# Optimization experiments

Hardware: AMD Instinct MI355X
Metric: run time of the kernel (lower is better)

The kernel has to match this reference:

```python
import jax, jax.numpy as jnp
import numpy as np

NUM_RBF = 16
TOP_K = 30
LOWER = 0.0
UPPER = 20.0
MAX_REL = 32  # PositionalEncodings max_relative_feature


def layer_norm(x, g, b, eps=1e-5):
    m = jnp.mean(x, -1, keepdims=True)
    v = jnp.var(x, -1, keepdims=True)
    return (x - m) / jnp.sqrt(v + eps) * g + b


def rbf(D):
    # exp(-((D - mu)/sigma)^2), mu = linspace(LOWER, UPPER, NUM_RBF)
    mu = jnp.linspace(LOWER, UPPER, NUM_RBF)
    sigma = (UPPER - LOWER) / NUM_RBF
    return jnp.exp(-(((D[..., None] - mu) / sigma) ** 2))


def setup_inputs() -> dict:
    key = jax.random.key(0)
    ks = jax.random.split(key, 6)
    B, L, A = 1, 1536, 14
    x = jax.random.normal(ks[0], (B, L, A, 3), jnp.float32) * 5.0
    S = jax.random.randint(ks[1], (B, L), 0, 21)
    mask = jnp.ones((B, L), jnp.float32)
    atom14_mask = jnp.ones((B, L, A), jnp.float32)
    R_idx = jnp.broadcast_to(jnp.arange(L, dtype=jnp.int32), (B, L))
    chain_labels = jnp.zeros((B, L), jnp.int32)
    protein_mpnn_feat = jax.random.normal(ks[2], (B, L, 128), jnp.float32)
    W_pos = jax.random.normal(ks[3], (2 * MAX_REL + 2, 16), jnp.float32) * 0.12
    b_pos = jnp.zeros((16,), jnp.float32)
    W_edge = jax.random.normal(ks[4], (16 + NUM_RBF * 14 * 14, 128), jnp.float32) * 0.018
    gamma_e = jnp.ones((128,), jnp.float32)
    beta_e = jnp.zeros((128,), jnp.float32)
    W_node = jax.random.normal(ks[5], (21 + 128, 128), jnp.float32) * 0.08
    gamma_n = jnp.ones((128,), jnp.float32)
    beta_n = jnp.zeros((128,), jnp.float32)
    return dict(x=x, mask=mask, atom14_mask=atom14_mask,
                protein_mpnn_feat=protein_mpnn_feat,
                W_pos=W_pos, b_pos=b_pos, W_edge=W_edge, gamma_e=gamma_e,
                beta_e=beta_e, W_node=W_node, gamma_n=gamma_n, beta_n=beta_n,
                S=S, R_idx=R_idx, chain_labels=chain_labels)


def reference(x, mask, atom14_mask, protein_mpnn_feat,
              W_pos, b_pos, W_edge, gamma_e, beta_e,
              W_node, gamma_n, beta_n, S, R_idx, chain_labels):
    B, L, A, _ = x.shape  # A = 14
    X_m = atom14_mask * mask[:, :, None]          # [B,L,14]
    Ca = x[:, :, 1]                                # CA_idx = 1

    # ---- _dist: masked pairwise CA distances + kNN topk (smallest) ----
    m2 = mask[:, None, :] * mask[:, :, None]       # [B,L,L]
    dX = Ca[:, None, :, :] - Ca[:, :, None, :]
    D = m2 * jnp.sqrt(jnp.sum(dX ** 2, -1) + 1e-6)
    D_max = jnp.max(D, -1, keepdims=True)
    D_adjust = D + (1.0 - m2) * D_max
    _, E_idx = jax.lax.top_k(-D_adjust, TOP_K)     # [B,L,K] smallest distances

    bidx = jnp.arange(B)[:, None, None]
    # gather neighbor atom coords / masks (all_coords_list == x in atom14 order)
    Xg = x[bidx, E_idx]                            # [B,L,K,14,3]
    Xm_g = X_m[bidx, E_idx]                        # [B,L,K,14]

    # ---- 14x14 pairwise atom RBFs to neighbors, fused/vectorized ----
    # Dp[b,l,k,i,j] = ||x[b,l,i] - x[b,E_idx[b,l,k],j]||
    Dp = jnp.sqrt(jnp.sum((x[:, :, None, :, None, :] - Xg[:, :, :, None, :, :]) ** 2, -1) + 1e-6)
    R = rbf(Dp)                                    # [B,L,K,14,14,16]
    R = R * X_m[:, :, None, :, None, None] * Xm_g[:, :, :, None, :, None]
    # torch loop cats atom_1-major, atom_2, then rbf bins -> same as reshape
    RBF_all = R.reshape(B, L, TOP_K, A * A * NUM_RBF)  # [B,L,K,3136]

    # ---- positional encodings ----
    offset = R_idx[:, :, None] - R_idx[:, None, :]           # [B,L,L]
    offset_g = jnp.take_along_axis(offset, E_idx, axis=2)    # [B,L,K]
    d_chains = (chain_labels[:, :, None] == chain_labels[:, None, :]).astype(jnp.int32)
    E_chains = jnp.take_along_axis(d_chains, E_idx, axis=2)  # [B,L,K]
    d = jnp.clip(offset_g + MAX_REL, 0, 2 * MAX_REL) * E_chains \
        + (1 - E_chains) * (2 * MAX_REL + 1)
    E_pos = jax.nn.one_hot(d, 2 * MAX_REL + 2, dtype=x.dtype) @ W_pos + b_pos

    # ---- edge embedding ----
    E = jnp.concatenate([E_pos, RBF_all], -1) @ W_edge       # [B,L,K,128]
    E = layer_norm(E, gamma_e, beta_e)

    # ---- node embedding ----
    V = jnp.concatenate([jax.nn.one_hot(S, 21, dtype=x.dtype), protein_mpnn_feat], -1) @ W_node
    V = layer_norm(V, gamma_n, beta_n)

    return (V, E, E_idx, x)
```

## Files before the change

### kernel.cpp

```cpp
#include <hip/hip_runtime.h>
#include <hip/hip_bf16.h>
#include <hip/hip_fp16.h>
#include <math.h>

#define LL 1536
#define NA 14
#define TOPK 30
#define KDIM 3152
#define KPAD 3200
#define NCHUNK 50

#define TOPK_BLKS 384
#define CONV_BLKS 100
#define NODE_BLKS 384
#define PREP_BLKS (TOPK_BLKS + CONV_BLKS + NODE_BLKS)

#define EDGE_BLKS 768

typedef __attribute__((ext_vector_type(8))) short bf16x8;
typedef __attribute__((ext_vector_type(4))) float f32x4;

static __device__ __forceinline__ float fexp2(float f) {
    return __builtin_amdgcn_exp2f(f);
}

static __device__ __forceinline__ unsigned cvt_pk_bf16(float lo, float hi) {
    unsigned r;
    asm("v_cvt_pk_bf16_f32 %0, %1, %2" : "=v"(r) : "v"(lo), "v"(hi));
    return r;
}

static __device__ __forceinline__ unsigned long long u64min(
    unsigned long long a, unsigned long long b) { return a < b ? a : b; }
static __device__ __forceinline__ unsigned long long u64max(
    unsigned long long a, unsigned long long b) { return a < b ? b : a; }

#define ASYNC16(ldsp, gp)                                                     \
    __builtin_amdgcn_global_load_lds(                                         \
        (const __attribute__((address_space(1))) void*)(gp),                  \
        (__attribute__((address_space(3))) void*)(ldsp), 16, 0, 0)

static __device__ __forceinline__ void build_rbf(
    ushort* dst, float4 xi4, float4 xj4,
    const float (&cA)[7], const float (&cB)[7])
{
    float dx = xi4.x - xj4.x, dy = xi4.y - xj4.y, dz = xi4.z - xj4.z;
    float dd = sqrtf(dx * dx + dy * dy + dz * dz + 1e-6f);
    dd = fminf(dd, 27.f);
    float coef = xi4.w * xj4.w;
    float w = fexp2(dd * 2.46219921f);
    float ev[16];
    float s8 = dd - 10.66666667f;
    ev[0] = fexp2(-0.92332483f * dd * dd) * coef;
    ev[8] = fexp2(-0.92332483f * s8 * s8) * coef;
    #pragma unroll
    for (int j = 1; j <= 7; ++j) {
        ev[j]     = ev[j - 1]     * w * cA[j - 1];
        ev[8 + j] = ev[8 + j - 1] * w * cB[j - 1];
    }
    union { unsigned u[8]; uint4 q[2]; } o;
    #pragma unroll
    for (int c = 0; c < 8; ++c) o.u[c] = cvt_pk_bf16(ev[2 * c], ev[2 * c + 1]);
    *(uint4*)&dst[0] = o.q[0];
    *(uint4*)&dst[8] = o.q[1];
}

__global__ __launch_bounds__(256) void prep_kernel(
    const float* __restrict__ x, const float* __restrict__ mask,
    const float* __restrict__ feat,
    const float* __restrict__ W_edge, ushort* __restrict__ Wt,
    const float* __restrict__ W_node, const float* __restrict__ gamma_n,
    const float* __restrict__ beta_n, const int* __restrict__ S,
    float* __restrict__ V, float* __restrict__ out_idx, float* __restrict__ out_x)
{
    __shared__ __align__(16) char sm[24576];
    const int blk = blockIdx.x;
    const int tid = threadIdx.x;

    if (blk < TOPK_BLKS) {
        float* ca  = (float*)sm;
        float* msk = (float*)sm + 4608;
        for (int t = tid; t < LL; t += 256) {
            msk[t] = mask[t];
            ca[t * 3 + 0] = x[t * 42 + 3];
            ca[t * 3 + 1] = x[t * 42 + 4];
            ca[t * 3 + 2] = x[t * 42 + 5];
        }
        __syncthreads();

        const int lane = tid & 63;
        const int i = blk * 4 + (tid >> 6);
        const float cix = ca[i * 3 + 0], ciy = ca[i * 3 + 1], ciz = ca[i * 3 + 2];
        const float mi = msk[i];

        float d[24], m2a[24];
        float lmax = 0.f;
        #pragma unroll
        for (int c = 0; c < 24; ++c) {
            int j = lane + c * 64;
            float dx = ca[j * 3 + 0] - cix;
            float dy = ca[j * 3 + 1] - ciy;
            float dz = ca[j * 3 + 2] - ciz;
            float m2 = mi * msk[j];
            float D = m2 * sqrtf(dx * dx + dy * dy + dz * dz + 1e-6f);
            d[c] = D; m2a[c] = m2;
            lmax = fmaxf(lmax, D);
        }
        #pragma unroll
        for (int m = 1; m < 64; m <<= 1) lmax = fmaxf(lmax, __shfl_xor(lmax, m));

        unsigned long long key[24];
        #pragma unroll
        for (int c = 0; c < 24; ++c) {
            float adj = d[c] + (1.f - m2a[c]) * lmax;
            key[c] = ((unsigned long long)__float_as_uint(adj) << 32)
                   | (unsigned)(lane + c * 64);
        }

        for (int t = 0; t < TOPK; t += 2) {
            unsigned long long p[12], q[12];
            #pragma unroll
            for (int c = 0; c < 12; ++c) {
                unsigned long long a = key[2 * c], b = key[2 * c + 1];
                p[c] = u64min(a, b); q[c] = u64max(a, b);
            }
            #pragma unroll
            for (int c = 0; c < 6; ++c) {
                unsigned long long hp = u64min(p[2 * c], p[2 * c + 1]);
                unsigned long long hq = u64min(u64max(p[2 * c], p[2 * c + 1]),
                                               u64min(q[2 * c], q[2 * c + 1]));
                p[c] = hp; q[c] = hq;
            }
            #pragma unroll
            for (int c = 0; c < 3; ++c) {
                unsigned long long hp = u64min(p[2 * c], p[2 * c + 1]);
                unsigned long long hq = u64min(u64max(p[2 * c], p[2 * c + 1]),
                                               u64min(q[2 * c], q[2 * c + 1]));
                p[c] = hp; q[c] = hq;
            }
            unsigned long long P = u64min(p[0], p[1]);
            unsigned long long Q = u64min(u64max(p[0], p[1]), u64min(q[0], q[1]));
            unsigned long long P2 = u64min(P, p[2]);
            unsigned long long Q2 = u64min(u64max(P, p[2]), u64min(Q, q[2]));
            #pragma unroll
            for (int m = 1; m < 64; m <<= 1) {
                unsigned long long op = __shfl_xor(P2, m);
                unsigned long long oq = __shfl_xor(Q2, m);
                unsigned long long np = u64min(P2, op);
                unsigned long long nq = u64min(u64max(P2, op), u64min(Q2, oq));
                P2 = np; Q2 = nq;
            }
            if (lane == 0) {
                out_idx[i * TOPK + t]     = (float)(unsigned)(P2 & 0xffffffffu);
                out_idx[i * TOPK + t + 1] = (float)(unsigned)(Q2 & 0xffffffffu);
            }
            #pragma unroll
            for (int c = 0; c < 24; ++c)
                if (key[c] == P2 || key[c] == Q2) key[c] = ~0ull;
        }
        for (int t = lane; t < 42; t += 64) out_x[i * 42 + t] = x[i * 42 + t];

    } else if (blk < TOPK_BLKS + CONV_BLKS) {
        int cb = blk - TOPK_BLKS;
        int k0 = (cb % 50) * 64, n0 = (cb / 50) * 64;
        float (*tile)[65] = (float (*)[65])sm;
        #pragma unroll
        for (int r = 0; r < 16; ++r) {
            int idx = r * 256 + tid;
            int kl = idx >> 6, nl = idx & 63;
            int k = k0 + kl;
            tile[nl][kl] = (k < KDIM) ? W_edge[k * 128 + n0 + nl] : 0.f;
        }
        __syncthreads();
        #pragma unroll
        for (int r = 0; r < 8; ++r) {
            int idx = r * 256 + tid;
            int nl = idx >> 5, kp = (idx & 31) * 2;
            unsigned pk = cvt_pk_bf16(tile[nl][kp], tile[nl][kp + 1]);
            *(unsigned*)&Wt[(size_t)(n0 + nl) * KPAD + k0 + kp] = pk;
        }

    } else {
        int nb = blk - TOPK_BLKS - CONV_BLKS;
        float* f = (float*)sm;
        const int w = tid >> 6, lane = tid & 63;
        const int i = nb * 4 + w;
        f[w * 128 + lane] = feat[i * 128 + lane];
        f[w * 128 + 64 + lane] = feat[i * 128 + 64 + lane];
        __syncthreads();
        int s = S[i];
        float a0 = W_node[s * 128 + lane];
        float a1 = W_node[s * 128 + 64 + lane];
        #pragma unroll 8
        for (int c = 0; c < 128; ++c) {
            float fc = f[w * 128 + c];
            a0 = fmaf(fc, W_node[(21 + c) * 128 + lane], a0);
            a1 = fmaf(fc, W_node[(21 + c) * 128 + 64 + lane], a1);
        }
        float ss = a0 + a1, qq = a0 * a0 + a1 * a1;
        #pragma unroll
        for (int m = 1; m < 64; m <<= 1) {
            ss += __shfl_xor(ss, m);
            qq += __shfl_xor(qq, m);
        }
        float mean = ss * (1.f / 128.f);
        float var = qq * (1.f / 128.f) - mean * mean;
        float inv = 1.f / sqrtf(var + 1e-5f);
        V[i * 128 + lane]      = (a0 - mean) * inv * gamma_n[lane] + beta_n[lane];
        V[i * 128 + 64 + lane] = (a1 - mean) * inv * gamma_n[64 + lane] + beta_n[64 + lane];
    }
}

__global__ __launch_bounds__(256, 3) void edge_mfma_kernel(
    const float* __restrict__ x, const float* __restrict__ mask,
    const float* __restrict__ a14m, const float* __restrict__ W_pos,
    const float* __restrict__ b_pos, const ushort* __restrict__ Wt,
    const float* __restrict__ gamma, const float* __restrict__ beta,
    const int* __restrict__ R_idx, const int* __restrict__ chain,
    const float* __restrict__ idxf, float* __restrict__ E)
{
    __shared__ __align__(16) ushort Bs[128 * 64];
    __shared__ __align__(16) ushort As[64 * 72];
    __shared__ __align__(16) float4 xjr[64][14];
    __shared__ __align__(16) float4 xir[2][14];
    __shared__ int   jl[64];
    __shared__ float lnS[64][2];
    __shared__ float lnQ[64][2];

    const int i0 = blockIdx.x * 2;
    const int tid = threadIdx.x;
    const int wave = tid >> 6, lane = tid & 63;

    if (tid < 64) {
        int g = tid >> 5, e = tid & 31;
        jl[tid] = (e < TOPK) ? (int)idxf[(i0 + g) * TOPK + e] : 0;
    } else if (tid < 64 + 28) {
        int t = tid - 64, g = t / 14, a = t - g * 14;
        const float* xp = &x[(i0 + g) * 42 + a * 3];
        xir[g][a] = make_float4(xp[0], xp[1], xp[2],
                                a14m[(i0 + g) * 14 + a] * mask[i0 + g]);
    }
    __syncthreads();

    for (int t = tid; t < 64 * 14; t += 256) {
        int row = t / 14, a = t - row * 14;
        int e = row & 31, j = jl[row];
        const float* xp = &x[j * 42 + a * 3];
        float mj = (e < TOPK) ? a14m[j * 14 + a] * mask[j] : 0.f;
        xjr[row][a] = make_float4(xp[0], xp[1], xp[2], mj);
    }
    __syncthreads();

    const int l16 = lane & 15, lk = lane >> 4, lk8 = lk * 8;
    const int mh = wave >> 1, nh = wave & 1;
    const int arow0 = (mh * 32 + l16) * 72, arow1 = arow0 + 16 * 72;
    const int row_b = tid >> 2, slot = tid & 3;
    const int gb = row_b >> 5, eb = row_b & 31;
    ushort* bdst = &As[row_b * 72 + slot * 16];

    float cA[7], cB[7];
    #pragma unroll
    for (int j = 1; j <= 7; ++j) {
        cA[j - 1] = __expf(-1.13777778f * (float)(2 * j - 1));
        cB[j - 1] = __expf(-1.13777778f * (float)(2 * (j + 8) - 1));
    }

    const int srow = wave * 32 + (lane >> 3);
    const int sseg = (lane & 7) ^ ((lane >> 3) & 7);
    const ushort* gsrc = Wt + (size_t)srow * KPAD + sseg * 8;

    #pragma unroll
    for (int it = 0; it < 4; ++it)
        ASYNC16(Bs + wave * 2048 + it * 512, gsrc + (size_t)it * 8 * KPAD);

    if (slot == 0) {
        float v[16];
        if (eb < TOPK) {
            int i = i0 + gb, j = jl[row_b];
            int off = R_idx[i] - R_idx[j];
            int ec = (chain[i] == chain[j]) ? 1 : 0;
            int dc = off + 32; dc = dc < 0 ? 0 : (dc > 64 ? 64 : dc);
            int d = ec ? dc : 65;
            #pragma unroll
            for (int c = 0; c < 16; ++c) v[c] = W_pos[d * 16 + c] + b_pos[c];
        } else {
            #pragma unroll
            for (int c = 0; c < 16; ++c) v[c] = 0.f;
        }
        union { unsigned u[8]; uint4 q[2]; } o;
        #pragma unroll
        for (int c = 0; c < 8; ++c) o.u[c] = cvt_pk_bf16(v[2 * c], v[2 * c + 1]);
        *(uint4*)&bdst[0] = o.q[0];
        *(uint4*)&bdst[8] = o.q[1];
    } else {
        build_rbf(bdst, xir[gb][0], xjr[row_b][slot - 1], cA, cB);
    }

    int boff[2][4];
    #pragma unroll
    for (int ks = 0; ks < 2; ++ks)
        #pragma unroll
        for (int nf = 0; nf < 4; ++nf) {
            int n = nh * 64 + nf * 16 + l16;
            boff[ks][nf] = n * 64 + ((((ks << 2) | lk) ^ (n & 7)) << 3);
        }

    int p = slot + 3, a1 = 0, a2 = slot + 3;
    f32x4 acc[2][4] = {};

    __syncthreads();

    for (int ch = 0; ch < NCHUNK; ++ch) {
        bf16x8 afr[2][2], bfr[2][4];
        #pragma unroll
        for (int ks = 0; ks < 2; ++ks) {
            afr[ks][0] = *(const bf16x8*)&As[arow0 + ks * 32 + lk8];
            afr[ks][1] = *(const bf16x8*)&As[arow1 + ks * 32 + lk8];
            #pragma unroll
            for (int nf = 0; nf < 4; ++nf)
                bfr[ks][nf] = *(const bf16x8*)&Bs[boff[ks][nf]];
        }
        __syncthreads();

        if (ch + 1 < NCHUNK) {
            #pragma unroll
            for (int it = 0; it < 4; ++it)
                ASYNC16(Bs + wave * 2048 + it * 512,
                        gsrc + (size_t)it * 8 * KPAD + (ch + 1) * 64);
            if (p <= 195) {
                build_rbf(bdst, xir[gb][a1], xjr[row_b][a2], cA, cB);
            } else {
                uint4 z = {0u, 0u, 0u, 0u};
                *(uint4*)&bdst[0] = z;
                *(uint4*)&bdst[8] = z;
            }
            p += 4; a2 += 4; if (a2 >= 14) { a2 -= 14; ++a1; }
        }

        #pragma unroll
        for (int ks = 0; ks < 2; ++ks)
            #pragma unroll
            for (int mf = 0; mf < 2; ++mf)
                #pragma unroll
                for (int nf = 0; nf < 4; ++nf)
                    acc[mf][nf] = __builtin_amdgcn_mfma_f32_16x16x32_bf16(
                        afr[ks][mf], bfr[ks][nf], acc[mf][nf], 0, 0, 0);

        __syncthreads();
    }

    #pragma unroll
    for (int mf = 0; mf < 2; ++mf)
        #pragma unroll
        for (int reg = 0; reg < 4; ++reg) {
            float s = acc[mf][0][reg] + acc[mf][1][reg] + acc[mf][2][reg] + acc[mf][3][reg];
            float q = acc[mf][0][reg] * acc[mf][0][reg] + acc[mf][1][reg] * acc[mf][1][reg]
                    + acc[mf][2][reg] * acc[mf][2][reg] + acc[mf][3][reg] * acc[mf][3][reg];
            #pragma unroll
            for (int m = 1; m < 16; m <<= 1) {
                s += __shfl_xor(s, m);
                q += __shfl_xor(q, m);
            }
            if (l16 == 0) {
                int row = mh * 32 + mf * 16 + lk * 4 + reg;
                lnS[row][nh] = s;
                lnQ[row][nh] = q;
            }
        }
    __syncthreads();

    float gl[4], bl[4];
    #pragma unroll
    for (int nf = 0; nf < 4; ++nf) {
        int col = nh * 64 + nf * 16 + l16;
        gl[nf] = gamma[col];
        bl[nf] = beta[col];
    }
    #pragma unroll
    for (int mf = 0; mf < 2; ++mf)
        #pragma unroll
        for (int reg = 0; reg < 4; ++reg) {
            int r = mh * 32 + mf * 16 + lk * 4 + reg;
            int e = r & 31, g = r >> 5;
            if (e < TOPK) {
                float s = lnS[r][0] + lnS[r][1];
                float q = lnQ[r][0] + lnQ[r][1];
                float mean = s * (1.f / 128.f);
                float var = q * (1.f / 128.f) - mean * mean;
                float inv = 1.f / sqrtf(var + 1e-5f);
                float* dst = &E[((size_t)((i0 + g) * TOPK + e)) * 128];
                #pragma unroll
                for (int nf = 0; nf < 4; ++nf) {
                    int col = nh * 64 + nf * 16 + l16;
                    dst[col] = (acc[mf][nf][reg] - mean) * inv * gl[nf] + bl[nf];
                }
            }
        }
}

extern "C" void kernel_launch(void* const* d_in, const int* in_sizes, int n_in,
                              void* d_out, int out_size, void* d_ws, size_t ws_size,
                              hipStream_t stream)
{
    const float* x       = (const float*)d_in[0];
    const float* mask    = (const float*)d_in[1];
    const float* a14m    = (const float*)d_in[2];
    const float* feat    = (const float*)d_in[3];
    const float* W_pos   = (const float*)d_in[4];
    const float* b_pos   = (const float*)d_in[5];
    const float* W_edge  = (const float*)d_in[6];
    const float* gamma_e = (const float*)d_in[7];
    const float* beta_e  = (const float*)d_in[8];
    const float* W_node  = (const float*)d_in[9];
    const float* gamma_n = (const float*)d_in[10];
    const float* beta_n  = (const float*)d_in[11];
    const int*   S       = (const int*)d_in[12];
    const int*   R_idx   = (const int*)d_in[13];
    const int*   chain   = (const int*)d_in[14];

    float* out     = (float*)d_out;
    float* V       = out;
    float* E       = out + 196608;
    float* out_idx = out + 196608 + 5898240;
    float* out_x   = out_idx + 46080;

    ushort* Wt = (ushort*)d_ws;

    prep_kernel<<<PREP_BLKS, 256, 0, stream>>>(
        x, mask, feat, W_edge, Wt, W_node, gamma_n, beta_n, S, V, out_idx, out_x);
    edge_mfma_kernel<<<EDGE_BLKS, 256, 0, stream>>>(
        x, mask, a14m, W_pos, b_pos, Wt, gamma_e, beta_e, R_idx, chain,
        out_idx, E);
}
```

Measured before the change: 102.4 us.

## Process three residues per edge block to amortize weight tile loads

Result: slower. 114.1 us (+11.5%).

```diff
diff --git a/kernel.cpp b/kernel.cpp
--- a/kernel.cpp
+++ b/kernel.cpp
@@ -15,7 +15,7 @@
 #define NODE_BLKS 384
 #define PREP_BLKS (TOPK_BLKS + CONV_BLKS + NODE_BLKS)
 
-#define EDGE_BLKS 768
+#define EDGE_BLKS 512
 
 typedef __attribute__((ext_vector_type(8))) short bf16x8;
 typedef __attribute__((ext_vector_type(4))) float f32x4;
@@ -211,7 +211,7 @@
     }
 }
 
-__global__ __launch_bounds__(256, 3) void edge_mfma_kernel(
+__global__ __launch_bounds__(256, 2) void edge_mfma_kernel(
     const float* __restrict__ x, const float* __restrict__ mask,
     const float* __restrict__ a14m, const float* __restrict__ W_pos,
     const float* __restrict__ b_pos, const ushort* __restrict__ Wt,
@@ -220,29 +220,29 @@
     const float* __restrict__ idxf, float* __restrict__ E)
 {
     __shared__ __align__(16) ushort Bs[128 * 64];
-    __shared__ __align__(16) ushort As[64 * 72];
-    __shared__ __align__(16) float4 xjr[64][14];
-    __shared__ __align__(16) float4 xir[2][14];
-    __shared__ int   jl[64];
-    __shared__ float lnS[64][2];
-    __shared__ float lnQ[64][2];
-
-    const int i0 = blockIdx.x * 2;
+    __shared__ __align__(16) ushort As[96 * 72];
+    __shared__ __align__(16) float4 xjr[96][14];
+    __shared__ __align__(16) float4 xir[3][14];
+    __shared__ int   jl[96];
+    __shared__ float lnS[96][2];
+    __shared__ float lnQ[96][2];
+
+    const int i0 = blockIdx.x * 3;
     const int tid = threadIdx.x;
     const int wave = tid >> 6, lane = tid & 63;
 
-    if (tid < 64) {
+    if (tid < 96) {
         int g = tid >> 5, e = tid & 31;
         jl[tid] = (e < TOPK) ? (int)idxf[(i0 + g) * TOPK + e] : 0;
-    } else if (tid < 64 + 28) {
-        int t = tid - 64, g = t / 14, a = t - g * 14;
+    } else if (tid < 96 + 42) {
+        int t = tid - 96, g = t / 14, a = t - g * 14;
         const float* xp = &x[(i0 + g) * 42 + a * 3];
         xir[g][a] = make_float4(xp[0], xp[1], xp[2],
                                 a14m[(i0 + g) * 14 + a] * mask[i0 + g]);
     }
     __syncthreads();
 
-    for (int t = tid; t < 64 * 14; t += 256) {
+    for (int t = tid; t < 96 * 14; t += 256) {
         int row = t / 14, a = t - row * 14;
         int e = row & 31, j = jl[row];
         const float* xp = &x[j * 42 + a * 3];
@@ -253,10 +253,9 @@
 
     const int l16 = lane & 15, lk = lane >> 4, lk8 = lk * 8;
     const int mh = wave >> 1, nh = wave & 1;
-    const int arow0 = (mh * 32 + l16) * 72, arow1 = arow0 + 16 * 72;
-    const int row_b = tid >> 2, slot = tid & 3;
-    const int gb = row_b >> 5, eb = row_b & 31;
-    ushort* bdst = &As[row_b * 72 + slot * 16];
+    const int row0 = tid >> 2, slot = tid & 3;
+    const int row1 = row0 + 64;
+    const int gb0 = row0 >> 5;
 
     float cA[7], cB[7];
     #pragma unroll
@@ -273,27 +272,38 @@
     for (int it = 0; it < 4; ++it)
         ASYNC16(Bs + wave * 2048 + it * 512, gsrc + (size_t)it * 8 * KPAD);
 
-    if (slot == 0) {
-        float v[16];
-        if (eb < TOPK) {
-            int i = i0 + gb, j = jl[row_b];
-            int off = R_idx[i] - R_idx[j];
-            int ec = (chain[i] == chain[j]) ? 1 : 0;
-            int dc = off + 32; dc = dc < 0 ? 0 : (dc > 64 ? 64 : dc);
-            int d = ec ? dc : 65;
-            #pragma unroll
-            for (int c = 0; c < 16; ++c) v[c] = W_pos[d * 16 + c] + b_pos[c];
-        } else {
-            #pragma unroll
-            for (int c = 0; c < 16; ++c) v[c] = 0.f;
-        }
-        union { unsigned u[8]; uint4 q[2]; } o;
-        #pragma unroll
-        for (int c = 0; c < 8; ++c) o.u[c] = cvt_pk_bf16(v[2 * c], v[2 * c + 1]);
-        *(uint4*)&bdst[0] = o.q[0];
-        *(uint4*)&bdst[8] = o.q[1];
-    } else {
-        build_rbf(bdst, xir[gb][0], xjr[row_b][slot - 1], cA, cB);
+    {
+        int row = row0, g = gb0;
+        #pragma unroll
+        for (int ps = 0; ps < 2; ++ps) {
+            if (ps == 0 || tid < 128) {
+                ushort* bd = &As[row * 72 + slot * 16];
+                if (slot == 0) {
+                    float v[16];
+                    int e = row & 31;
+                    if (e < TOPK) {
+                        int i = i0 + g, j = jl[row];
+                        int off = R_idx[i] - R_idx[j];
+                        int ec = (chain[i] == chain[j]) ? 1 : 0;
+                        int dc = off + 32; dc = dc < 0 ? 0 : (dc > 64 ? 64 : dc);
+                        int d = ec ? dc : 65;
+                        #pragma unroll
+                        for (int c = 0; c < 16; ++c) v[c] = W_pos[d * 16 + c] + b_pos[c];
+                    } else {
+                        #pragma unroll
+                        for (int c = 0; c < 16; ++c) v[c] = 0.f;
+                    }
+                    union { unsigned u[8]; uint4 q[2]; } o;
+                    #pragma unroll
+                    for (int c = 0; c < 8; ++c) o.u[c] = cvt_pk_bf16(v[2 * c], v[2 * c + 1]);
+                    *(uint4*)&bd[0] = o.q[0];
+                    *(uint4*)&bd[8] = o.q[1];
+                } else {
+                    build_rbf(bd, xir[g][0], xjr[row][slot - 1], cA, cB);
+                }
+            }
+            row = row1; g = 2;
+        }
     }
 
     int boff[2][4];
@@ -304,18 +314,23 @@
             int n = nh * 64 + nf * 16 + l16;
             boff[ks][nf] = n * 64 + ((((ks << 2) | lk) ^ (n & 7)) << 3);
         }
+    int aoff[3];
+    #pragma unroll
+    for (int mf = 0; mf < 3; ++mf)
+        aoff[mf] = (mh * 48 + mf * 16 + l16) * 72;
 
     int p = slot + 3, a1 = 0, a2 = slot + 3;
-    f32x4 acc[2][4] = {};
+    f32x4 acc[3][4] = {};
 
     __syncthreads();
 
     for (int ch = 0; ch < NCHUNK; ++ch) {
-        bf16x8 afr[2][2], bfr[2][4];
+        bf16x8 afr[2][3], bfr[2][4];
         #pragma unroll
         for (int ks = 0; ks < 2; ++ks) {
-            afr[ks][0] = *(const bf16x8*)&As[arow0 + ks * 32 + lk8];
-            afr[ks][1] = *(const bf16x8*)&As[arow1 + ks * 32 + lk8];
+            #pragma unroll
+            for (int mf = 0; mf < 3; ++mf)
+                afr[ks][mf] = *(const bf16x8*)&As[aoff[mf] + ks * 32 + lk8];
             #pragma unroll
             for (int nf = 0; nf < 4; ++nf)
                 bfr[ks][nf] = *(const bf16x8*)&Bs[boff[ks][nf]];
@@ -327,12 +342,20 @@
             for (int it = 0; it < 4; ++it)
                 ASYNC16(Bs + wave * 2048 + it * 512,
                         gsrc + (size_t)it * 8 * KPAD + (ch + 1) * 64);
-            if (p <= 195) {
-                build_rbf(bdst, xir[gb][a1], xjr[row_b][a2], cA, cB);
-            } else {
-                uint4 z = {0u, 0u, 0u, 0u};
-                *(uint4*)&bdst[0] = z;
-                *(uint4*)&bdst[8] = z;
+            int row = row0, g = gb0;
+            #pragma unroll
+            for (int ps = 0; ps < 2; ++ps) {
+                if (ps == 0 || tid < 128) {
+                    ushort* bd = &As[row * 72 + slot * 16];
+                    if (p <= 195) {
+                        build_rbf(bd, xir[g][a1], xjr[row][a2], cA, cB);
+                    } else {
+                        uint4 z = {0u, 0u, 0u, 0u};
+                        *(uint4*)&bd[0] = z;
+                        *(uint4*)&bd[8] = z;
+                    }
+                }
+                row = row1; g = 2;
             }
             p += 4; a2 += 4; if (a2 >= 14) { a2 -= 14; ++a1; }
         }
@@ -340,7 +363,7 @@
         #pragma unroll
         for (int ks = 0; ks < 2; ++ks)
             #pragma unroll
-            for (int mf = 0; mf < 2; ++mf)
+            for (int mf = 0; mf < 3; ++mf)
                 #pragma unroll
                 for (int nf = 0; nf < 4; ++nf)
                     acc[mf][nf] = __builtin_amdgcn_mfma_f32_16x16x32_bf16(
@@ -350,7 +373,7 @@
     }
 
     #pragma unroll
-    for (int mf = 0; mf < 2; ++mf)
+    for (int mf = 0; mf < 3; ++mf)
         #pragma unroll
         for (int reg = 0; reg < 4; ++reg) {
             float s = acc[mf][0][reg] + acc[mf][1][reg] + acc[mf][2][reg] + acc[mf][3][reg];
@@ -362,7 +385,7 @@
                 q += __shfl_xor(q, m);
             }
             if (l16 == 0) {
-                int row = mh * 32 + mf * 16 + lk * 4 + reg;
+                int row = mh * 48 + mf * 16 + lk * 4 + reg;
                 lnS[row][nh] = s;
                 lnQ[row][nh] = q;
             }
@@ -377,10 +400,10 @@
         bl[nf] = beta[col];
     }
     #pragma unroll
-    for (int mf = 0; mf < 2; ++mf)
+    for (int mf = 0; mf < 3; ++mf)
         #pragma unroll
         for (int reg = 0; reg < 4; ++reg) {
-            int r = mh * 32 + mf * 16 + lk * 4 + reg;
+            int r = mh * 48 + mf * 16 + lk * 4 + reg;
             int e = r & 31, g = r >> 5;
             if (e < TOPK) {
                 float s = lnS[r][0] + lnS[r][1];
```

## Load edge weight fragments directly from global into registers, drop LDS staging

Applied to the files above, without the earlier changes.

Result: slower. 184.3 us (+80.0%).

```diff
diff --git a/kernel.cpp b/kernel.cpp
--- a/kernel.cpp
+++ b/kernel.cpp
@@ -34,11 +34,6 @@
     unsigned long long a, unsigned long long b) { return a < b ? a : b; }
 static __device__ __forceinline__ unsigned long long u64max(
     unsigned long long a, unsigned long long b) { return a < b ? b : a; }
-
-#define ASYNC16(ldsp, gp)                                                     \
-    __builtin_amdgcn_global_load_lds(                                         \
-        (const __attribute__((address_space(1))) void*)(gp),                  \
-        (__attribute__((address_space(3))) void*)(ldsp), 16, 0, 0)
 
 static __device__ __forceinline__ void build_rbf(
     ushort* dst, float4 xi4, float4 xj4,
@@ -219,7 +214,6 @@
     const int* __restrict__ R_idx, const int* __restrict__ chain,
     const float* __restrict__ idxf, float* __restrict__ E)
 {
-    __shared__ __align__(16) ushort Bs[128 * 64];
     __shared__ __align__(16) ushort As[64 * 72];
     __shared__ __align__(16) float4 xjr[64][14];
     __shared__ __align__(16) float4 xir[2][14];
@@ -265,13 +259,10 @@
         cB[j - 1] = __expf(-1.13777778f * (float)(2 * (j + 8) - 1));
     }
 
-    const int srow = wave * 32 + (lane >> 3);
-    const int sseg = (lane & 7) ^ ((lane >> 3) & 7);
-    const ushort* gsrc = Wt + (size_t)srow * KPAD + sseg * 8;
-
-    #pragma unroll
-    for (int it = 0; it < 4; ++it)
-        ASYNC16(Bs + wave * 2048 + it * 512, gsrc + (size_t)it * 8 * KPAD);
+    const ushort* bp0 = Wt + (size_t)(nh * 64 +  0 + l16) * KPAD + lk8;
+    const ushort* bp1 = Wt + (size_t)(nh * 64 + 16 + l16) * KPAD + lk8;
+    const ushort* bp2 = Wt + (size_t)(nh * 64 + 32 + l16) * KPAD + lk8;
+    const ushort* bp3 = Wt + (size_t)(nh * 64 + 48 + l16) * KPAD + lk8;
 
     if (slot == 0) {
         float v[16];
@@ -296,37 +287,33 @@
         build_rbf(bdst, xir[gb][0], xjr[row_b][slot - 1], cA, cB);
     }
 
-    int boff[2][4];
-    #pragma unroll
-    for (int ks = 0; ks < 2; ++ks)
-        #pragma unroll
-        for (int nf = 0; nf < 4; ++nf) {
-            int n = nh * 64 + nf * 16 + l16;
-            boff[ks][nf] = n * 64 + ((((ks << 2) | lk) ^ (n & 7)) << 3);
-        }
-
     int p = slot + 3, a1 = 0, a2 = slot + 3;
     f32x4 acc[2][4] = {};
 
     __syncthreads();
 
     for (int ch = 0; ch < NCHUNK; ++ch) {
-        bf16x8 afr[2][2], bfr[2][4];
-        #pragma unroll
-        for (int ks = 0; ks < 2; ++ks) {
-            afr[ks][0] = *(const bf16x8*)&As[arow0 + ks * 32 + lk8];
-            afr[ks][1] = *(const bf16x8*)&As[arow1 + ks * 32 + lk8];
-            #pragma unroll
-            for (int nf = 0; nf < 4; ++nf)
-                bfr[ks][nf] = *(const bf16x8*)&Bs[boff[ks][nf]];
-        }
-        __syncthreads();
+        bf16x8 bfr[2][4];
+        asm volatile("global_load_dwordx4 %0, %1, off"           : "=v"(bfr[0][0]) : "v"(bp0));
+        asm volatile("global_load_dwordx4 %0, %1, off offset:64" : "=v"(bfr[1][0]) : "v"(bp0));
+        asm volatile("global_load_dwordx4 %0, %1, off"           : "=v"(bfr[0][1]) : "v"(bp1));
+        asm volatile("global_load_dwordx4 %0, %1, off offset:64" : "=v"(bfr[1][1]) : "v"(bp1));
+        asm volatile("global_load_dwordx4 %0, %1, off"           : "=v"(bfr[0][2]) : "v"(bp2));
+        asm volatile("global_load_dwordx4 %0, %1, off offset:64" : "=v"(bfr[1][2]) : "v"(bp2));
+        asm volatile("global_load_dwordx4 %0, %1, off"           : "=v"(bfr[0][3]) : "v"(bp3));
+        asm volatile("global_load_dwordx4 %0, %1, off offset:64" : "=v"(bfr[1][3]) : "v"(bp3));
+
+        bf16x8 afr[2][2];
+        afr[0][0] = *(const bf16x8*)&As[arow0 + lk8];
+        afr[0][1] = *(const bf16x8*)&As[arow1 + lk8];
+        afr[1][0] = *(const bf16x8*)&As[arow0 + 32 + lk8];
+        afr[1][1] = *(const bf16x8*)&As[arow1 + 32 + lk8];
+
+        asm volatile("s_waitcnt lgkmcnt(0)" ::: "memory");
+        __builtin_amdgcn_sched_barrier(0);
+        __builtin_amdgcn_s_barrier();
 
         if (ch + 1 < NCHUNK) {
-            #pragma unroll
-            for (int it = 0; it < 4; ++it)
-                ASYNC16(Bs + wave * 2048 + it * 512,
-                        gsrc + (size_t)it * 8 * KPAD + (ch + 1) * 64);
             if (p <= 195) {
                 build_rbf(bdst, xir[gb][a1], xjr[row_b][a2], cA, cB);
             } else {
@@ -337,6 +324,8 @@
             p += 4; a2 += 4; if (a2 >= 14) { a2 -= 14; ++a1; }
         }
 
+        asm volatile("s_waitcnt vmcnt(0)" ::: "memory");
+        __builtin_amdgcn_sched_barrier(0);
         #pragma unroll
         for (int ks = 0; ks < 2; ++ks)
             #pragma unroll
@@ -346,7 +335,11 @@
                     acc[mf][nf] = __builtin_amdgcn_mfma_f32_16x16x32_bf16(
                         afr[ks][mf], bfr[ks][nf], acc[mf][nf], 0, 0, 0);
 
-        __syncthreads();
+        asm volatile("s_waitcnt lgkmcnt(0)" ::: "memory");
+        __builtin_amdgcn_sched_barrier(0);
+        __builtin_amdgcn_s_barrier();
+
+        bp0 += 64; bp1 += 64; bp2 += 64; bp3 += 64;
     }
 
     #pragma unroll
```
